# Kernel tuning notes

Hardware: AMD Instinct MI355X
Metric: run time of the kernel (lower is better)

Reference implementation:

```python
import jax, jax.numpy as jnp
import numpy as np

B = 4_000_000

# physical constants from initBatteryParams
R_ = 8.3144621
F_ = 96487.0
ALPHA = 0.5
SN = 0.0002
SP = 0.0002
KN = 20000.0
KP = 20000.0
VOL = 2.2e-05
VOLS = 0.1 * VOL
VOLB = VOL - VOLS
TO = 10.0
TSN = 90.0
TSP = 90.0
U0P = 4.03
U0N = 0.01
QMAX_BASE = 10000.0
RO_BASE = 10.0
T_DIFFUSION = 7.0e6  # repo default; attribute used in getNextState
DT = 1.0


def setup_inputs() -> dict:
    key = jax.random.key(0)
    ks = jax.random.split(key, 12)
    qMax = 1.4 * jnp.ones((B,), jnp.float32)   # 14000/qMaxBASE
    Ro = 0.015 * jnp.ones((B,), jnp.float32)   # 0.15/RoBASE
    # physically plausible initial state (get_initial_state) + small noise
    qM = qMax * QMAX_BASE  # [B]
    Tb = 292.1 + 0.5 * jax.random.normal(ks[0], (B, 1), jnp.float32)
    Vo = 0.01 * jax.random.uniform(ks[1], (B, 1), jnp.float32)
    Vsn = 0.01 * jax.random.uniform(ks[2], (B, 1), jnp.float32)
    Vsp = 0.01 * jax.random.uniform(ks[3], (B, 1), jnp.float32)
    jitter = lambda k: 1.0 + 0.01 * jax.random.normal(k, (B, 1), jnp.float32)
    qnB = (qM * 0.6 * VOLB / VOL)[:, None] * jitter(ks[4])
    qnS = (qM * 0.6 * VOLS / VOL)[:, None] * jitter(ks[5])
    qpB = (qM * 0.4 * VOLB / VOL)[:, None] * jitter(ks[6])
    qpS = (qM * 0.4 * VOLS / VOL)[:, None] * jitter(ks[7])
    states = jnp.concatenate([Tb, Vo, Vsn, Vsp, qnB, qnS, qpB, qpS], axis=1)
    inputs = 1.0 + 2.0 * jax.random.uniform(ks[8], (B, 1), jnp.float32)  # current [A]
    kw = jax.random.split(ks[9], 8)
    return {
        "inputs": inputs, "states": states, "qMax": qMax, "Ro": Ro,
        "Wp0": 0.5 * jax.random.normal(kw[0], (8, 1), jnp.float32),
        "bp0": 0.1 * jax.random.normal(kw[1], (8,), jnp.float32),
        "Wp2": 0.5 * jax.random.normal(kw[2], (4, 8), jnp.float32),
        "bp2": 0.1 * jax.random.normal(kw[3], (4,), jnp.float32),
        "Wp4": 0.5 * jax.random.normal(kw[4], (1, 4), jnp.float32),
        "bp4": 0.1 * jax.random.normal(kw[5], (1,), jnp.float32),
        "Wn": 0.0016 * jnp.ones((1, 1), jnp.float32),  # ~fitted Linear(1,1)
        "bn": -0.0008 * jnp.ones((1,), jnp.float32),
    }


def _mlp_p(x, Wp0, bp0, Wp2, bp2, Wp4, bp4):
    h = jnp.tanh(x @ Wp0.T + bp0)
    h = jnp.tanh(h @ Wp2.T + bp2)
    return h @ Wp4.T + bp4


def _cell(inputs, states, qMax, Ro, Wp0, bp0, Wp2, bp2, Wp4, bp4, Wn, bn):
    Tb, Vo, Vsn, Vsp, qnB, qnS, qpB, qpS = jnp.split(states, 8, axis=1)
    i = inputs  # [B,1]
    qSMax = (qMax * QMAX_BASE * VOLS / VOL)[:, None]  # [B,1]
    # --- getNextState ---
    xpS = jnp.clip(qpS / qSMax, 1e-18, 1.0)
    xnS = jnp.clip(qnS / qSMax, 1e-18, 1.0)
    Jn0 = 1e-18 + KN * (1.0 - xnS) ** ALPHA * xnS ** ALPHA
    Jp0 = 1e-18 + KP * (1.0 - xpS) ** ALPHA * xpS ** ALPHA
    qdotDiffusionBSn = (qnB / VOLB - qnS / VOLS) / T_DIFFUSION
    qdotDiffusionBSp = (qpB / VOLB - qpS / VOLS) / T_DIFFUSION
    Jn = i / SN
    Jp = i / SP
    VoNominal = i * Ro[:, None] * RO_BASE
    VsnNominal = R_ * Tb / F_ / ALPHA * jnp.arcsinh(Jn / (2.0 * Jn0))
    VspNominal = R_ * Tb / F_ / ALPHA * jnp.arcsinh(Jp / (2.0 * Jp0))
    Tb2 = Tb  # Tbdot = 0
    Vo2 = Vo + (VoNominal - Vo) / TO * DT
    Vsn2 = Vsn + (VsnNominal - Vsn) / TSN * DT
    Vsp2 = Vsp + (VspNominal - Vsp) / TSP * DT
    qnB2 = qnB + (-qdotDiffusionBSn) * DT
    qnS2 = qnS + (qdotDiffusionBSn - i) * DT
    qpB2 = qpB + (-qdotDiffusionBSp) * DT
    qpS2 = qpS + (i + qdotDiffusionBSp) * DT
    XNew = jnp.concatenate([Tb2, Vo2, Vsn2, Vsp2, qnB2, qnS2, qpB2, qpS2], axis=1)
    # --- getNextOutput (on XNew) ---
    xpS_o = qpS2 / qSMax
    xnS_o = qnS2 / qSMax
    VepMLP = _mlp_p(xpS_o, Wp0, bp0, Wp2, bp2, Wp4, bp4)
    VenMLP = xnS_o @ Wn.T + bn
    safe_log_p = jnp.clip((1.0 - xpS_o) / xpS_o, 1e-18, 1e18)
    safe_log_n = jnp.clip((1.0 - xnS_o) / xnS_o, 1e-18, 1e18)
    Vep = U0P + R_ * Tb2 / F_ * jnp.log(safe_log_p) + VepMLP
    Ven = U0N + R_ * Tb2 / F_ * jnp.log(safe_log_n) + VenMLP
    V = Vep - Ven - Vo2 - Vsn2 - Vsp2
    return V, XNew


def reference(inputs, states, qMax, Ro, Wp0, bp0, Wp2, bp2, Wp4, bp4, Wn, bn):
    return _cell(inputs, states, qMax, Ro, Wp0, bp0, Wp2, bp2, Wp4, bp4, Wn, bn)
```

## Files before the change

kernel.cpp:

```cpp
#include <hip/hip_runtime.h>
#include <math.h>

typedef float v4f __attribute__((ext_vector_type(4)));
typedef float v2f __attribute__((ext_vector_type(2)));

#define RTF       (8.3144621f / 96487.0f)
#define VOLS_     2.2e-06f
#define VOLB_     1.98e-05f
#define INV_TDIFF (1.0f / 7.0e6f)

#define LUT_N 4096
#define ROWS  8

__device__ __forceinline__ float asinh_pos(float x) {
    return __logf(x + sqrtf(fmaf(x, x, 1.0f)));
}

__device__ __forceinline__ float jval(float x) {
    float j0 = 1e-18f + 20000.0f * sqrtf(fmaxf(x * (1.0f - x), 0.0f));
    return 1.0f / (2.0f * j0);
}

__device__ __forceinline__ void mlp_log_eval(
    float x,
    const float* __restrict__ Wp0, const float* __restrict__ bp0,
    const float* __restrict__ Wp2, const float* __restrict__ bp2,
    const float* __restrict__ Wp4, const float* __restrict__ bp4,
    float* mlp_out, float* log_out)
{
    float h1[8];
#pragma unroll
    for (int j = 0; j < 8; j++)
        h1[j] = tanhf(fmaf(x, Wp0[j], bp0[j]));
    float mlp = bp4[0];
#pragma unroll
    for (int k = 0; k < 4; k++) {
        float a = bp2[k];
#pragma unroll
        for (int j = 0; j < 8; j++)
            a = fmaf(h1[j], Wp2[k * 8 + j], a);
        mlp = fmaf(tanhf(a), Wp4[k], mlp);
    }
    *mlp_out = mlp;
    float r = fminf(fmaxf((1.0f - x) / fmaxf(x, 1e-30f), 1e-18f), 1e18f);
    *log_out = RTF * logf(r);
}

__global__ __launch_bounds__(256) void build_lut_kernel(
    const float* __restrict__ Wp0, const float* __restrict__ bp0,
    const float* __restrict__ Wp2, const float* __restrict__ bp2,
    const float* __restrict__ Wp4, const float* __restrict__ bp4,
    v2f* __restrict__ lutJ2, v4f* __restrict__ lutO4)
{
    int idx = blockIdx.x * blockDim.x + threadIdx.x;
    if (idx >= LUT_N) return;
    const float dx = 1.0f / (float)(LUT_N - 1);
    float x0 = (float)idx * dx;
    float x1 = fminf(x0 + dx, 1.0f);

    v2f j; j.x = jval(x0); j.y = jval(x1);
    lutJ2[idx] = j;

    float m0, l0, m1, l1;
    mlp_log_eval(x0, Wp0, bp0, Wp2, bp2, Wp4, bp4, &m0, &l0);
    mlp_log_eval(x1, Wp0, bp0, Wp2, bp2, Wp4, bp4, &m1, &l1);
    v4f o; o.x = m0; o.y = l0; o.z = m1; o.w = l1;
    lutO4[idx] = o;
}

struct Row { v4f s0, s1; float i, qm, ro; };

__device__ __forceinline__ Row load_row(
    const float* __restrict__ inp, const v4f* __restrict__ st4,
    const float* __restrict__ qMaxp, const float* __restrict__ Rop, int b)
{
    Row r;
    r.s0 = st4[2 * b];
    r.s1 = st4[2 * b + 1];
    r.i  = inp[b];
    r.qm = qMaxp[b];
    r.ro = Rop[b];
    return r;
}

__device__ __forceinline__ void process_row(
    int b, const Row& r, float wn, float wbn,
    const v2f* __restrict__ lutJ2, const v4f* __restrict__ lutO4,
    float* __restrict__ outV, v4f* __restrict__ ox4)
{
    float Tb  = r.s0.x, Vo  = r.s0.y, Vsn = r.s0.z, Vsp = r.s0.w;
    float qnB = r.s1.x, qnS = r.s1.y, qpB = r.s1.z, qpS = r.s1.w;
    float i   = r.i;

    float invq = __fdividef(1.0f, r.qm * 1000.0f);

    float xpS = fminf(fmaxf(qpS * invq, 1e-18f), 1.0f);
    float xnS = fminf(fmaxf(qnS * invq, 1e-18f), 1.0f);

    float tn = xnS * (float)(LUT_N - 1);
    float tp = xpS * (float)(LUT_N - 1);
    int in0 = min((int)tn, LUT_N - 2);
    int ip0 = min((int)tp, LUT_N - 2);
    float fn = tn - (float)in0;
    float fp = tp - (float)ip0;
    v2f jn = lutJ2[in0];
    v2f jp = lutJ2[ip0];
    float inv2Jn = fmaf(fn, jn.y - jn.x, jn.x);
    float inv2Jp = fmaf(fp, jp.y - jp.x, jp.x);

    float qdotn = (qnB * (1.0f / VOLB_) - qnS * (1.0f / VOLS_)) * INV_TDIFF;
    float qdotp = (qpB * (1.0f / VOLB_) - qpS * (1.0f / VOLS_)) * INV_TDIFF;

    float Jn   = i * 5000.0f;
    float VoNom  = i * r.ro * 10.0f;
    float coef   = RTF * Tb * 2.0f;
    float VsnNom = coef * asinh_pos(Jn * inv2Jn);
    float VspNom = coef * asinh_pos(Jn * inv2Jp);

    float Vo2  = Vo  + (VoNom  - Vo ) * 0.1f;
    float Vsn2 = Vsn + (VsnNom - Vsn) * (1.0f / 90.0f);
    float Vsp2 = Vsp + (VspNom - Vsp) * (1.0f / 90.0f);
    float qnB2 = qnB - qdotn;
    float qnS2 = qnS + qdotn - i;
    float qpB2 = qpB - qdotp;
    float qpS2 = qpS + i + qdotp;

    float xp = qpS2 * invq;
    float xn = qnS2 * invq;

    float tpo = fminf(fmaxf(xp, 0.0f), 1.0f) * (float)(LUT_N - 1);
    float tno = fminf(fmaxf(xn, 0.0f), 1.0f) * (float)(LUT_N - 1);
    int ipo = min((int)tpo, LUT_N - 2);
    int ino = min((int)tno, LUT_N - 2);
    float fpo = tpo - (float)ipo;
    float fno = tno - (float)ino;
    v4f op = lutO4[ipo];
    v4f on = lutO4[ino];
    float mlp_p = fmaf(fpo, op.z - op.x, op.x);
    float log_p = fmaf(fpo, op.w - op.y, op.y);
    float log_n = fmaf(fno, on.w - on.y, on.y);

    float Vep = 4.03f + Tb * log_p + mlp_p;
    float Ven = 0.01f + Tb * log_n + fmaf(xn, wn, wbn);
    float V = Vep - Ven - Vo2 - Vsn2 - Vsp2;

    __builtin_nontemporal_store(V, &outV[b]);
    v4f o0; o0.x = Tb;   o0.y = Vo2;  o0.z = Vsn2; o0.w = Vsp2;
    v4f o1; o1.x = qnB2; o1.y = qnS2; o1.z = qpB2; o1.w = qpS2;
    __builtin_nontemporal_store(o0, &ox4[2 * b]);
    __builtin_nontemporal_store(o1, &ox4[2 * b + 1]);
}

__global__ __launch_bounds__(256) void battery_cell_kernel(
    const float* __restrict__ inp,
    const float* __restrict__ st,
    const float* __restrict__ qMaxp,
    const float* __restrict__ Rop,
    const float* __restrict__ Wn,
    const float* __restrict__ bn,
    const v2f*   __restrict__ lutJ2,
    const v4f*   __restrict__ lutO4,
    float* __restrict__ outV,
    float* __restrict__ outX,
    int B)
{
    const v4f* st4 = (const v4f*)st;
    v4f* ox4 = (v4f*)outX;
    float wn = Wn[0], wbn = bn[0];

    int base = blockIdx.x * (256 * ROWS) + threadIdx.x;

    if (base + (ROWS - 1) * 256 < B) {
        Row cur = load_row(inp, st4, qMaxp, Rop, base);
#pragma unroll
        for (int k = 0; k < ROWS; k++) {
            Row nxt;
            if (k + 1 < ROWS)
                nxt = load_row(inp, st4, qMaxp, Rop, base + (k + 1) * 256);
            process_row(base + k * 256, cur, wn, wbn, lutJ2, lutO4, outV, ox4);
            if (k + 1 < ROWS)
                cur = nxt;
        }
    } else {
        for (int k = 0; k < ROWS; k++) {
            int b = base + k * 256;
            if (b < B) {
                Row r = load_row(inp, st4, qMaxp, Rop, b);
                process_row(b, r, wn, wbn, lutJ2, lutO4, outV, ox4);
            }
        }
    }
}

extern "C" void kernel_launch(void* const* d_in, const int* in_sizes, int n_in,
                              void* d_out, int out_size, void* d_ws, size_t ws_size,
                              hipStream_t stream) {
    const float* inp  = (const float*)d_in[0];
    const float* st   = (const float*)d_in[1];
    const float* qMax = (const float*)d_in[2];
    const float* Ro   = (const float*)d_in[3];
    const float* Wp0  = (const float*)d_in[4];
    const float* bp0  = (const float*)d_in[5];
    const float* Wp2  = (const float*)d_in[6];
    const float* bp2  = (const float*)d_in[7];
    const float* Wp4  = (const float*)d_in[8];
    const float* bp4  = (const float*)d_in[9];
    const float* Wn   = (const float*)d_in[10];
    const float* bn   = (const float*)d_in[11];

    int B = in_sizes[0];
    float* outV = (float*)d_out;
    float* outX = (float*)d_out + B;

    v2f* lutJ2 = (v2f*)d_ws;
    v4f* lutO4 = (v4f*)((char*)d_ws + LUT_N * 8);

    build_lut_kernel<<<LUT_N / 256, 256, 0, stream>>>(
        Wp0, bp0, Wp2, bp2, Wp4, bp4, lutJ2, lutO4);

    int chunk = 256 * ROWS;
    int grid = (B + chunk - 1) / chunk;
    battery_cell_kernel<<<grid, 256, 0, stream>>>(
        inp, st, qMax, Ro, Wn, bn, lutJ2, lutO4, outV, outX, B);
}
```

Baseline: 312.0 us.

## Assign contiguous rows per thread with vectorized loads and stores

```diff
diff --git a/kernel.cpp b/kernel.cpp
--- a/kernel.cpp
+++ b/kernel.cpp
@@ -10,7 +10,7 @@
 #define INV_TDIFF (1.0f / 7.0e6f)
 
 #define LUT_N 4096
-#define ROWS  8
+#define ROWS  4
 
 __device__ __forceinline__ float asinh_pos(float x) {
     return __logf(x + sqrtf(fmaf(x, x, 1.0f)));
@@ -68,31 +68,15 @@
     lutO4[idx] = o;
 }
 
-struct Row { v4f s0, s1; float i, qm, ro; };
-
-__device__ __forceinline__ Row load_row(
-    const float* __restrict__ inp, const v4f* __restrict__ st4,
-    const float* __restrict__ qMaxp, const float* __restrict__ Rop, int b)
-{
-    Row r;
-    r.s0 = st4[2 * b];
-    r.s1 = st4[2 * b + 1];
-    r.i  = inp[b];
-    r.qm = qMaxp[b];
-    r.ro = Rop[b];
-    return r;
-}
-
 __device__ __forceinline__ void process_row(
-    int b, const Row& r, float wn, float wbn,
+    float Tb, float Vo, float Vsn, float Vsp,
+    float qnB, float qnS, float qpB, float qpS,
+    float i, float qm, float ro,
+    float wn, float wbn,
     const v2f* __restrict__ lutJ2, const v4f* __restrict__ lutO4,
-    float* __restrict__ outV, v4f* __restrict__ ox4)
-{
-    float Tb  = r.s0.x, Vo  = r.s0.y, Vsn = r.s0.z, Vsp = r.s0.w;
-    float qnB = r.s1.x, qnS = r.s1.y, qpB = r.s1.z, qpS = r.s1.w;
-    float i   = r.i;
-
-    float invq = __fdividef(1.0f, r.qm * 1000.0f);
+    float& Vout, v4f& o0, v4f& o1)
+{
+    float invq = __fdividef(1.0f, qm * 1000.0f);
 
     float xpS = fminf(fmaxf(qpS * invq, 1e-18f), 1.0f);
     float xnS = fminf(fmaxf(qnS * invq, 1e-18f), 1.0f);
@@ -111,8 +95,8 @@
     float qdotn = (qnB * (1.0f / VOLB_) - qnS * (1.0f / VOLS_)) * INV_TDIFF;
     float qdotp = (qpB * (1.0f / VOLB_) - qpS * (1.0f / VOLS_)) * INV_TDIFF;
 
-    float Jn   = i * 5000.0f;
-    float VoNom  = i * r.ro * 10.0f;
+    float Jn     = i * 5000.0f;
+    float VoNom  = i * ro * 10.0f;
     float coef   = RTF * Tb * 2.0f;
     float VsnNom = coef * asinh_pos(Jn * inv2Jn);
     float VspNom = coef * asinh_pos(Jn * inv2Jp);
@@ -142,13 +126,10 @@
 
     float Vep = 4.03f + Tb * log_p + mlp_p;
     float Ven = 0.01f + Tb * log_n + fmaf(xn, wn, wbn);
-    float V = Vep - Ven - Vo2 - Vsn2 - Vsp2;
-
-    __builtin_nontemporal_store(V, &outV[b]);
-    v4f o0; o0.x = Tb;   o0.y = Vo2;  o0.z = Vsn2; o0.w = Vsp2;
-    v4f o1; o1.x = qnB2; o1.y = qnS2; o1.z = qpB2; o1.w = qpS2;
-    __builtin_nontemporal_store(o0, &ox4[2 * b]);
-    __builtin_nontemporal_store(o1, &ox4[2 * b + 1]);
+    Vout = Vep - Ven - Vo2 - Vsn2 - Vsp2;
+
+    o0.x = Tb;   o0.y = Vo2;  o0.z = Vsn2; o0.w = Vsp2;
+    o1.x = qnB2; o1.y = qnS2; o1.z = qpB2; o1.w = qpS2;
 }
 
 __global__ __launch_bounds__(256) void battery_cell_kernel(
@@ -164,30 +145,56 @@
     float* __restrict__ outX,
     int B)
 {
-    const v4f* st4 = (const v4f*)st;
-    v4f* ox4 = (v4f*)outX;
+    int t = blockIdx.x * blockDim.x + threadIdx.x;
+    int base = t * ROWS;
+    if (base >= B) return;
+
     float wn = Wn[0], wbn = bn[0];
 
-    int base = blockIdx.x * (256 * ROWS) + threadIdx.x;
-
-    if (base + (ROWS - 1) * 256 < B) {
-        Row cur = load_row(inp, st4, qMaxp, Rop, base);
-#pragma unroll
-        for (int k = 0; k < ROWS; k++) {
-            Row nxt;
-            if (k + 1 < ROWS)
-                nxt = load_row(inp, st4, qMaxp, Rop, base + (k + 1) * 256);
-            process_row(base + k * 256, cur, wn, wbn, lutJ2, lutO4, outV, ox4);
-            if (k + 1 < ROWS)
-                cur = nxt;
+    if (base + ROWS <= B) {
+        v4f vi = *(const v4f*)(inp   + base);
+        v4f vq = *(const v4f*)(qMaxp + base);
+        v4f vr = *(const v4f*)(Rop   + base);
+        v4f s[8];
+        const v4f* stp = (const v4f*)st + 2 * base;
+#pragma unroll
+        for (int k = 0; k < 8; k++) s[k] = stp[k];
+
+        v4f ov;
+        v4f ox[8];
+#pragma unroll
+        for (int r = 0; r < ROWS; r++) {
+            float V;
+            v4f o0, o1;
+            process_row(s[2 * r].x, s[2 * r].y, s[2 * r].z, s[2 * r].w,
+                        s[2 * r + 1].x, s[2 * r + 1].y, s[2 * r + 1].z, s[2 * r + 1].w,
+                        vi[r], vq[r], vr[r], wn, wbn, lutJ2, lutO4,
+                        V, o0, o1);
+            ov[r] = V;
+            ox[2 * r]     = o0;
+            ox[2 * r + 1] = o1;
         }
+
+        *(v4f*)(outV + base) = ov;
+        v4f* oxp = (v4f*)outX + 2 * base;
+#pragma unroll
+        for (int k = 0; k < 8; k++) oxp[k] = ox[k];
     } else {
-        for (int k = 0; k < ROWS; k++) {
-            int b = base + k * 256;
-            if (b < B) {
-                Row r = load_row(inp, st4, qMaxp, Rop, b);
-                process_row(b, r, wn, wbn, lutJ2, lutO4, outV, ox4);
-            }
+        for (int r = 0; r < ROWS; r++) {
+            int b = base + r;
+            if (b >= B) break;
+            const v4f* stp = (const v4f*)st;
+            v4f s0 = stp[2 * b];
+            v4f s1 = stp[2 * b + 1];
+            float V;
+            v4f o0, o1;
+            process_row(s0.x, s0.y, s0.z, s0.w, s1.x, s1.y, s1.z, s1.w,
+                        inp[b], qMaxp[b], Rop[b], wn, wbn, lutJ2, lutO4,
+                        V, o0, o1);
+            outV[b] = V;
+            v4f* oxp = (v4f*)outX;
+            oxp[2 * b]     = o0;
+            oxp[2 * b + 1] = o1;
         }
     }
 }
@@ -218,8 +225,8 @@
     build_lut_kernel<<<LUT_N / 256, 256, 0, stream>>>(
         Wp0, bp0, Wp2, bp2, Wp4, bp4, lutJ2, lutO4);
 
-    int chunk = 256 * ROWS;
-    int grid = (B + chunk - 1) / chunk;
+    int threads_needed = (B + ROWS - 1) / ROWS;
+    int grid = (threads_needed + 255) / 256;
     battery_cell_kernel<<<grid, 256, 0, stream>>>(
         inp, st, qMax, Ro, Wn, bn, lutJ2, lutO4, outV, outX, B);
 }
```

New measurement: 329.3 us. +5.6%, slower.

## Stage halved LUT in shared memory and process one row per thread

Applied to the files above, without the earlier changes.

```diff
diff --git a/kernel.cpp b/kernel.cpp
--- a/kernel.cpp
+++ b/kernel.cpp
@@ -9,8 +9,8 @@
 #define VOLB_     1.98e-05f
 #define INV_TDIFF (1.0f / 7.0e6f)
 
-#define LUT_N 4096
-#define ROWS  8
+#define LUT_N 2048
+#define BLOCK 512
 
 __device__ __forceinline__ float asinh_pos(float x) {
     return __logf(x + sqrtf(fmaf(x, x, 1.0f)));
@@ -68,31 +68,49 @@
     lutO4[idx] = o;
 }
 
-struct Row { v4f s0, s1; float i, qm, ro; };
-
-__device__ __forceinline__ Row load_row(
-    const float* __restrict__ inp, const v4f* __restrict__ st4,
-    const float* __restrict__ qMaxp, const float* __restrict__ Rop, int b)
+__global__ __launch_bounds__(BLOCK) void battery_cell_kernel(
+    const float* __restrict__ inp,
+    const float* __restrict__ st,
+    const float* __restrict__ qMaxp,
+    const float* __restrict__ Rop,
+    const float* __restrict__ Wn,
+    const float* __restrict__ bn,
+    const float* __restrict__ lutG,
+    float* __restrict__ outV,
+    float* __restrict__ outX,
+    int B)
 {
-    Row r;
-    r.s0 = st4[2 * b];
-    r.s1 = st4[2 * b + 1];
-    r.i  = inp[b];
-    r.qm = qMaxp[b];
-    r.ro = Rop[b];
-    return r;
-}
-
-__device__ __forceinline__ void process_row(
-    int b, const Row& r, float wn, float wbn,
-    const v2f* __restrict__ lutJ2, const v4f* __restrict__ lutO4,
-    float* __restrict__ outV, v4f* __restrict__ ox4)
-{
-    float Tb  = r.s0.x, Vo  = r.s0.y, Vsn = r.s0.z, Vsp = r.s0.w;
-    float qnB = r.s1.x, qnS = r.s1.y, qpB = r.s1.z, qpS = r.s1.w;
-    float i   = r.i;
-
-    float invq = __fdividef(1.0f, r.qm * 1000.0f);
+    __shared__ float slut[12288];
+
+    int b = blockIdx.x * BLOCK + threadIdx.x;
+
+    bool active = (b < B);
+    int bc = active ? b : 0;
+    const v4f* st4 = (const v4f*)st;
+    v4f s0 = st4[2 * bc];
+    v4f s1 = st4[2 * bc + 1];
+    float i  = inp[bc];
+    float qm = qMaxp[bc];
+    float ro = Rop[bc];
+    float wn = Wn[0], wbn = bn[0];
+
+    {
+        const v4f* src = (const v4f*)lutG;
+        v4f* dst = (v4f*)slut;
+#pragma unroll
+        for (int k = 0; k < 6; k++)
+            dst[threadIdx.x + k * BLOCK] = src[threadIdx.x + k * BLOCK];
+    }
+    __syncthreads();
+    const v2f* lutJ2 = (const v2f*)slut;
+    const v4f* lutO4 = (const v4f*)(slut + 4096);
+
+    if (!active) return;
+
+    float Tb  = s0.x, Vo  = s0.y, Vsn = s0.z, Vsp = s0.w;
+    float qnB = s1.x, qnS = s1.y, qpB = s1.z, qpS = s1.w;
+
+    float invq = __fdividef(1.0f, qm * 1000.0f);
 
     float xpS = fminf(fmaxf(qpS * invq, 1e-18f), 1.0f);
     float xnS = fminf(fmaxf(qnS * invq, 1e-18f), 1.0f);
@@ -111,8 +129,8 @@
     float qdotn = (qnB * (1.0f / VOLB_) - qnS * (1.0f / VOLS_)) * INV_TDIFF;
     float qdotp = (qpB * (1.0f / VOLB_) - qpS * (1.0f / VOLS_)) * INV_TDIFF;
 
-    float Jn   = i * 5000.0f;
-    float VoNom  = i * r.ro * 10.0f;
+    float Jn     = i * 5000.0f;
+    float VoNom  = i * ro * 10.0f;
     float coef   = RTF * Tb * 2.0f;
     float VsnNom = coef * asinh_pos(Jn * inv2Jn);
     float VspNom = coef * asinh_pos(Jn * inv2Jp);
@@ -144,52 +162,12 @@
     float Ven = 0.01f + Tb * log_n + fmaf(xn, wn, wbn);
     float V = Vep - Ven - Vo2 - Vsn2 - Vsp2;
 
-    __builtin_nontemporal_store(V, &outV[b]);
+    outV[b] = V;
     v4f o0; o0.x = Tb;   o0.y = Vo2;  o0.z = Vsn2; o0.w = Vsp2;
     v4f o1; o1.x = qnB2; o1.y = qnS2; o1.z = qpB2; o1.w = qpS2;
-    __builtin_nontemporal_store(o0, &ox4[2 * b]);
-    __builtin_nontemporal_store(o1, &ox4[2 * b + 1]);
-}
-
-__global__ __launch_bounds__(256) void battery_cell_kernel(
-    const float* __restrict__ inp,
-    const float* __restrict__ st,
-    const float* __restrict__ qMaxp,
-    const float* __restrict__ Rop,
-    const float* __restrict__ Wn,
-    const float* __restrict__ bn,
-    const v2f*   __restrict__ lutJ2,
-    const v4f*   __restrict__ lutO4,
-    float* __restrict__ outV,
-    float* __restrict__ outX,
-    int B)
-{
-    const v4f* st4 = (const v4f*)st;
     v4f* ox4 = (v4f*)outX;
-    float wn = Wn[0], wbn = bn[0];
-
-    int base = blockIdx.x * (256 * ROWS) + threadIdx.x;
-
-    if (base + (ROWS - 1) * 256 < B) {
-        Row cur = load_row(inp, st4, qMaxp, Rop, base);
-#pragma unroll
-        for (int k = 0; k < ROWS; k++) {
-            Row nxt;
-            if (k + 1 < ROWS)
-                nxt = load_row(inp, st4, qMaxp, Rop, base + (k + 1) * 256);
-            process_row(base + k * 256, cur, wn, wbn, lutJ2, lutO4, outV, ox4);
-            if (k + 1 < ROWS)
-                cur = nxt;
-        }
-    } else {
-        for (int k = 0; k < ROWS; k++) {
-            int b = base + k * 256;
-            if (b < B) {
-                Row r = load_row(inp, st4, qMaxp, Rop, b);
-                process_row(b, r, wn, wbn, lutJ2, lutO4, outV, ox4);
-            }
-        }
-    }
+    ox4[2 * b]     = o0;
+    ox4[2 * b + 1] = o1;
 }
 
 extern "C" void kernel_launch(void* const* d_in, const int* in_sizes, int n_in,
@@ -218,8 +196,7 @@
     build_lut_kernel<<<LUT_N / 256, 256, 0, stream>>>(
         Wp0, bp0, Wp2, bp2, Wp4, bp4, lutJ2, lutO4);
 
-    int chunk = 256 * ROWS;
-    int grid = (B + chunk - 1) / chunk;
-    battery_cell_kernel<<<grid, 256, 0, stream>>>(
-        inp, st, qMax, Ro, Wn, bn, lutJ2, lutO4, outV, outX, B);
-}
+    int grid = (B + BLOCK - 1) / BLOCK;
+    battery_cell_kernel<<<grid, BLOCK, 0, stream>>>(
+        inp, st, qMax, Ro, Wn, bn, (const float*)d_ws, outV, outX, B);
+}
```

Result: faster. 292.0 us (-6.4%).
